# Kernel optimization log

Hardware: AMD Instinct MI355X
Metric: run time of the kernel (lower is better)

The kernel has to match this reference:

```python
import jax, jax.numpy as jnp
import numpy as np

N, C = 8, 3
HD, WD = 1024, 1280   # camera (depth) resolution
HS, WS = 800, 1280    # projector pattern resolution


def _build_calib():
    fx, fy, dx, dy = 1200.0, 1200.0, 640.0, 512.0
    ww = np.arange(WD, dtype=np.float32)[None, :].repeat(HD, 0)
    hh = np.arange(HD, dtype=np.float32)[:, None].repeat(WD, 1)
    vec = np.stack([(ww - dx) / fx, (hh - dy) / fy, np.ones_like(ww)], axis=2)  # [H,W,3]
    th = 0.15
    ext_rot = np.array([[np.cos(th), 0.0, np.sin(th)],
                        [0.0, 1.0, 0.0],
                        [-np.sin(th), 0.0, np.cos(th)]], np.float32)
    abc = np.einsum('ij,hwj->hwi', ext_rot, vec).astype(np.float32)  # [H,W,3]
    abc_mat = np.transpose(abc, (2, 0, 1))  # [3,H,W] (plb.a2t HWC->CHW)
    ext_tran = np.array([200.0, 0.0, 50.0], np.float32)
    pat_intrin = np.array([1100.0, 1100.0, 640.0, 400.0], np.float32)
    return abc_mat, ext_tran, pat_intrin


def setup_inputs() -> dict:
    key = jax.random.key(0)
    k1, k2 = jax.random.split(key)
    abc, tr, pi = _build_calib()
    depth_mat = 500.0 + 500.0 * jax.random.uniform(k1, (N, 1, HD, WD), jnp.float32)
    src_mat = jax.random.normal(k2, (N, C, HS, WS), jnp.float32)
    return {"depth_mat": depth_mat, "src_mat": src_mat,
            "abc_mat": jnp.asarray(abc), "ext_tran": jnp.asarray(tr),
            "pat_intrin": jnp.asarray(pi)}


def _grid_sample_border(src, gx, gy):
    # src: [N,C,Hs,Ws]; gx,gy: [N,H,W] normalized grid; bilinear,
    # align_corners=False, padding_mode='border' (torch semantics).
    n, c, hs, ws = src.shape
    x = ((gx + 1.0) * ws - 1.0) * 0.5
    y = ((gy + 1.0) * hs - 1.0) * 0.5
    x = jnp.clip(x, 0.0, ws - 1.0)
    y = jnp.clip(y, 0.0, hs - 1.0)
    x0 = jnp.floor(x)
    y0 = jnp.floor(y)
    wx = x - x0
    wy = y - y0
    x0i = x0.astype(jnp.int32)
    y0i = y0.astype(jnp.int32)
    x1i = jnp.minimum(x0i + 1, ws - 1)
    y1i = jnp.minimum(y0i + 1, hs - 1)
    b = jnp.arange(n)[:, None, None]

    def g(yi, xi):
        return src[b, :, yi, xi]  # [N,H,W,C]

    out = (g(y0i, x0i) * ((1.0 - wy) * (1.0 - wx))[..., None]
           + g(y0i, x1i) * ((1.0 - wy) * wx)[..., None]
           + g(y1i, x0i) * (wy * (1.0 - wx))[..., None]
           + g(y1i, x1i) * (wy * wx)[..., None])
    return jnp.transpose(out, (0, 3, 1, 2))  # [N,C,H,W]


def reference(depth_mat, src_mat, abc_mat, ext_tran, pat_intrin):
    hs, ws = src_mat.shape[-2:]
    denom = abc_mat[2] * depth_mat + ext_tran[2]          # [N,1,H,W]
    xx = (abc_mat[0] * depth_mat + ext_tran[0]) / denom
    yy = (abc_mat[1] * depth_mat + ext_tran[1]) / denom
    fu, fv, du, dv = pat_intrin
    uu = fu * xx + du
    vv = fv * yy + dv
    # NOTE: original normalizes by (size-1) even with align_corners=False;
    # replicated faithfully.
    gx = 2.0 * uu[:, 0] / (ws - 1) - 1.0                  # [N,H,W]
    gy = 2.0 * vv[:, 0] / (hs - 1) - 1.0
    return _grid_sample_border(src_mat, gx, gy)
```

## Files before the change

kernel.cpp:

```cpp
#include <hip/hip_runtime.h>

#define N_  8
#define C_  3
#define HD_ 1024
#define WD_ 1280
#define HS_ 800
#define WS_ 1280

__global__ __launch_bounds__(256) void warp_from_depth_kernel(
    const float* __restrict__ depth,
    const float* __restrict__ src,
    const float* __restrict__ abc,
    const float* __restrict__ tr,
    const float* __restrict__ pin,
    float* __restrict__ out)
{
    const int HW = HD_ * WD_;
    int idx = blockIdx.x * blockDim.x + threadIdx.x;
    if (idx >= N_ * HW) return;

    int n  = idx / HW;
    int hw = idx - n * HW;

    float d = depth[idx];
    float a = abc[hw];
    float b = abc[HW + hw];
    float c = abc[2 * HW + hw];

    float tx = tr[0], ty = tr[1], tz = tr[2];
    float fu = pin[0], fv = pin[1], du = pin[2], dv = pin[3];

    float denom = c * d + tz;
    float inv = 1.0f / denom;
    float xx = (a * d + tx) * inv;
    float yy = (b * d + ty) * inv;
    float uu = fu * xx + du;
    float vv = fv * yy + dv;

    float gx = 2.0f * uu / (float)(WS_ - 1) - 1.0f;
    float gy = 2.0f * vv / (float)(HS_ - 1) - 1.0f;
    float x = ((gx + 1.0f) * (float)WS_ - 1.0f) * 0.5f;
    float y = ((gy + 1.0f) * (float)HS_ - 1.0f) * 0.5f;

    x = fminf(fmaxf(x, 0.0f), (float)(WS_ - 1));
    y = fminf(fmaxf(y, 0.0f), (float)(HS_ - 1));

    float x0f = floorf(x);
    float y0f = floorf(y);
    float wx = x - x0f;
    float wy = y - y0f;
    int x0 = (int)x0f;
    int y0 = (int)y0f;
    int x1 = min(x0 + 1, WS_ - 1);
    int y1 = min(y0 + 1, HS_ - 1);

    float w00 = (1.0f - wy) * (1.0f - wx);
    float w01 = (1.0f - wy) * wx;
    float w10 = wy * (1.0f - wx);
    float w11 = wy * wx;

    const size_t HWs = (size_t)HS_ * WS_;
    const float* sn = src + (size_t)n * C_ * HWs;
    int o00 = y0 * WS_ + x0;
    int o01 = y0 * WS_ + x1;
    int o10 = y1 * WS_ + x0;
    int o11 = y1 * WS_ + x1;

    float* on = out + (size_t)n * C_ * HW + hw;
#pragma unroll
    for (int ch = 0; ch < C_; ++ch) {
        const float* sc = sn + (size_t)ch * HWs;
        float v = sc[o00] * w00 + sc[o01] * w01
                + sc[o10] * w10 + sc[o11] * w11;
        on[(size_t)ch * HW] = v;
    }
}

extern "C" void kernel_launch(void* const* d_in, const int* in_sizes, int n_in,
                              void* d_out, int out_size, void* d_ws, size_t ws_size,
                              hipStream_t stream) {
    const float* depth = (const float*)d_in[0];
    const float* src   = (const float*)d_in[1];
    const float* abc   = (const float*)d_in[2];
    const float* tr    = (const float*)d_in[3];
    const float* pin   = (const float*)d_in[4];
    float* out = (float*)d_out;

    const int total = N_ * HD_ * WD_;
    const int block = 256;
    const int grid = (total + block - 1) / block;
    warp_from_depth_kernel<<<grid, block, 0, stream>>>(depth, src, abc, tr, pin, out);
}
```

Before: 347.2 us.

## Pre-pack source into interleaved bf16 channels before bilinear gather

Adds a pre-pass kernel that converts the planar fp32 source image into a per-pixel interleaved bf16 layout of 8 bytes per pixel, with the three channels packed into one uint2. The main warp kernel then fetches each of the four bilinear taps with a single 8-byte load instead of twelve scattered fp32 loads across three planes. This targets gather traffic and cache-line waste in the main kernel. In exchange it adds a full read of the source and a write of the packed copy on every call, and it lowers the precision of source values to bf16, which may break tolerance. A planar fallback runs when the workspace is too small.

Measured after the change: 316.0 us. 9.0% less time.

```diff
diff --git a/kernel.cpp b/kernel.cpp
--- a/kernel.cpp
+++ b/kernel.cpp
@@ -7,9 +7,47 @@
 #define HS_ 800
 #define WS_ 1280
 
-__global__ __launch_bounds__(256) void warp_from_depth_kernel(
+__device__ __forceinline__ unsigned short f2bf(float f) {
+    unsigned int u = __float_as_uint(f);
+    unsigned int r = (u + 0x7FFFu + ((u >> 16) & 1u)) >> 16;
+    return (unsigned short)r;
+}
+__device__ __forceinline__ float bf2f(unsigned int h) {
+    return __uint_as_float(h << 16);
+}
+
+__global__ __launch_bounds__(256) void interleave_kernel(
+    const float* __restrict__ src, uint4* __restrict__ ws)
+{
+    const size_t HWs = (size_t)HS_ * WS_;
+    size_t g = (size_t)blockIdx.x * blockDim.x + threadIdx.x;
+    size_t base = g * 4;
+    if (base >= (size_t)N_ * HWs) return;
+    int n = (int)(base / HWs);
+    size_t p = base - (size_t)n * HWs;
+    const float* s = src + (size_t)n * C_ * HWs + p;
+    float4 c0 = *(const float4*)(s);
+    float4 c1 = *(const float4*)(s + HWs);
+    float4 c2 = *(const float4*)(s + 2 * HWs);
+
+    uint4 A, B;
+    A.x = (unsigned)f2bf(c0.x) | ((unsigned)f2bf(c1.x) << 16);
+    A.y = (unsigned)f2bf(c2.x);
+    A.z = (unsigned)f2bf(c0.y) | ((unsigned)f2bf(c1.y) << 16);
+    A.w = (unsigned)f2bf(c2.y);
+    B.x = (unsigned)f2bf(c0.z) | ((unsigned)f2bf(c1.z) << 16);
+    B.y = (unsigned)f2bf(c2.z);
+    B.z = (unsigned)f2bf(c0.w) | ((unsigned)f2bf(c1.w) << 16);
+    B.w = (unsigned)f2bf(c2.w);
+
+    size_t o = base / 2;
+    ws[o]     = A;
+    ws[o + 1] = B;
+}
+
+__global__ __launch_bounds__(256) void warp_main_kernel(
     const float* __restrict__ depth,
-    const float* __restrict__ src,
+    const uint2* __restrict__ wsrc,
     const float* __restrict__ abc,
     const float* __restrict__ tr,
     const float* __restrict__ pin,
@@ -60,19 +98,67 @@
     float w11 = wy * wx;
 
     const size_t HWs = (size_t)HS_ * WS_;
+    const uint2* sn = wsrc + (size_t)n * HWs;
+    uint2 t00 = sn[(size_t)y0 * WS_ + x0];
+    uint2 t01 = sn[(size_t)y0 * WS_ + x1];
+    uint2 t10 = sn[(size_t)y1 * WS_ + x0];
+    uint2 t11 = sn[(size_t)y1 * WS_ + x1];
+
+    float* on = out + (size_t)n * C_ * HW + hw;
+
+    float v0 = bf2f(t00.x & 0xFFFFu) * w00 + bf2f(t01.x & 0xFFFFu) * w01
+             + bf2f(t10.x & 0xFFFFu) * w10 + bf2f(t11.x & 0xFFFFu) * w11;
+    float v1 = bf2f(t00.x >> 16) * w00 + bf2f(t01.x >> 16) * w01
+             + bf2f(t10.x >> 16) * w10 + bf2f(t11.x >> 16) * w11;
+    float v2 = bf2f(t00.y & 0xFFFFu) * w00 + bf2f(t01.y & 0xFFFFu) * w01
+             + bf2f(t10.y & 0xFFFFu) * w10 + bf2f(t11.y & 0xFFFFu) * w11;
+
+    on[0]              = v0;
+    on[(size_t)HW]     = v1;
+    on[(size_t)2 * HW] = v2;
+}
+
+__global__ __launch_bounds__(256) void warp_planar_kernel(
+    const float* __restrict__ depth, const float* __restrict__ src,
+    const float* __restrict__ abc, const float* __restrict__ tr,
+    const float* __restrict__ pin, float* __restrict__ out)
+{
+    const int HW = HD_ * WD_;
+    int idx = blockIdx.x * blockDim.x + threadIdx.x;
+    if (idx >= N_ * HW) return;
+    int n  = idx / HW;
+    int hw = idx - n * HW;
+    float d = depth[idx];
+    float a = abc[hw];
+    float b = abc[HW + hw];
+    float c = abc[2 * HW + hw];
+    float denom = c * d + tr[2];
+    float inv = 1.0f / denom;
+    float uu = pin[0] * ((a * d + tr[0]) * inv) + pin[2];
+    float vv = pin[1] * ((b * d + tr[1]) * inv) + pin[3];
+    float gx = 2.0f * uu / (float)(WS_ - 1) - 1.0f;
+    float gy = 2.0f * vv / (float)(HS_ - 1) - 1.0f;
+    float x = ((gx + 1.0f) * (float)WS_ - 1.0f) * 0.5f;
+    float y = ((gy + 1.0f) * (float)HS_ - 1.0f) * 0.5f;
+    x = fminf(fmaxf(x, 0.0f), (float)(WS_ - 1));
+    y = fminf(fmaxf(y, 0.0f), (float)(HS_ - 1));
+    float x0f = floorf(x), y0f = floorf(y);
+    float wx = x - x0f, wy = y - y0f;
+    int x0 = (int)x0f, y0 = (int)y0f;
+    int x1 = min(x0 + 1, WS_ - 1);
+    int y1 = min(y0 + 1, HS_ - 1);
+    float w00 = (1.0f - wy) * (1.0f - wx), w01 = (1.0f - wy) * wx;
+    float w10 = wy * (1.0f - wx), w11 = wy * wx;
+    const size_t HWs = (size_t)HS_ * WS_;
     const float* sn = src + (size_t)n * C_ * HWs;
-    int o00 = y0 * WS_ + x0;
-    int o01 = y0 * WS_ + x1;
-    int o10 = y1 * WS_ + x0;
-    int o11 = y1 * WS_ + x1;
-
+    int o00 = y0 * WS_ + x0, o01 = y0 * WS_ + x1;
+    int o10 = y1 * WS_ + x0, o11 = y1 * WS_ + x1;
     float* on = out + (size_t)n * C_ * HW + hw;
 #pragma unroll
     for (int ch = 0; ch < C_; ++ch) {
         const float* sc = sn + (size_t)ch * HWs;
-        float v = sc[o00] * w00 + sc[o01] * w01
-                + sc[o10] * w10 + sc[o11] * w11;
-        on[(size_t)ch * HW] = v;
+        on[(size_t)ch * HW] = sc[o00] * w00 + sc[o01] * w01
+                            + sc[o10] * w10 + sc[o11] * w11;
     }
 }
 
@@ -86,8 +172,19 @@
     const float* pin   = (const float*)d_in[4];
     float* out = (float*)d_out;
 
+    const size_t need = (size_t)N_ * HS_ * WS_ * 8;
     const int total = N_ * HD_ * WD_;
     const int block = 256;
-    const int grid = (total + block - 1) / block;
-    warp_from_depth_kernel<<<grid, block, 0, stream>>>(depth, src, abc, tr, pin, out);
+
+    if (ws_size >= need) {
+        const size_t src_px = (size_t)N_ * HS_ * WS_;
+        const int g1 = (int)((src_px / 4 + block - 1) / block);
+        interleave_kernel<<<g1, block, 0, stream>>>(src, (uint4*)d_ws);
+        const int g2 = (total + block - 1) / block;
+        warp_main_kernel<<<g2, block, 0, stream>>>(depth, (const uint2*)d_ws,
+                                                   abc, tr, pin, out);
+    } else {
+        const int g = (total + block - 1) / block;
+        warp_planar_kernel<<<g, block, 0, stream>>>(depth, src, abc, tr, pin, out);
+    }
 }
```

## Pack source into fp16 horizontal-pair texels and gather with dot2

Applied to the files above, without the earlier changes.

Adds a pre-pass that converts the planar fp32 source into an interleaved 16-byte texel holding fp16 pairs (x, x+1) for all three channels. The main kernel then needs only two 16-byte gathers per output pixel instead of twelve scalar loads, does the blend with fdot2, and handles four pixels per thread with vector loads and nontemporal stores. This cuts scattered gather transactions, but adds a full pass over the source into workspace each call and lowers precision to fp16 for source values and weights.

Result: faster. 339.4 us (-2.2%).

```diff
diff --git a/kernel.cpp b/kernel.cpp
--- a/kernel.cpp
+++ b/kernel.cpp
@@ -7,72 +7,175 @@
 #define HS_ 800
 #define WS_ 1280
 
-__global__ __launch_bounds__(256) void warp_from_depth_kernel(
+typedef _Float16 h2_t __attribute__((ext_vector_type(2)));
+typedef float f32x4 __attribute__((ext_vector_type(4)));
+
+__device__ __forceinline__ unsigned pack_h2(float a, float b) {
+    h2_t h;
+    h.x = (_Float16)a;
+    h.y = (_Float16)b;
+    return __builtin_bit_cast(unsigned, h);
+}
+__device__ __forceinline__ h2_t as_h2(unsigned u) {
+    return __builtin_bit_cast(h2_t, u);
+}
+__device__ __forceinline__ float fdot2(h2_t a, h2_t b, float c) {
+#if __has_builtin(__builtin_amdgcn_fdot2)
+    return __builtin_amdgcn_fdot2(a, b, c, false);
+#else
+    return (float)a.x * (float)b.x + (float)a.y * (float)b.y + c;
+#endif
+}
+
+__global__ __launch_bounds__(256) void pair_pack_kernel(
+    const float* __restrict__ src, uint4* __restrict__ ws)
+{
+    const size_t HWs = (size_t)HS_ * WS_;
+    size_t g = (size_t)blockIdx.x * blockDim.x + threadIdx.x;
+    if (g >= (size_t)N_ * HWs) return;
+    int n = (int)(g / HWs);
+    size_t p = g - (size_t)n * HWs;
+    int x = (int)(p % WS_);
+    int dx = (x < WS_ - 1) ? 1 : 0;
+
+    const float* s0 = src + (size_t)n * C_ * HWs + p;
+    const float* s1 = s0 + HWs;
+    const float* s2 = s1 + HWs;
+
+    float c0a = s0[0], c0b = s0[dx];
+    float c1a = s1[0], c1b = s1[dx];
+    float c2a = s2[0], c2b = s2[dx];
+
+    uint4 e;
+    e.x = pack_h2(c0a, c0b);
+    e.y = pack_h2(c1a, c1b);
+    e.z = pack_h2(c2a, c2b);
+    e.w = 0u;
+    ws[g] = e;
+}
+
+__global__ __launch_bounds__(256) void warp_main4_kernel(
     const float* __restrict__ depth,
-    const float* __restrict__ src,
+    const uint4* __restrict__ wsrc,
     const float* __restrict__ abc,
     const float* __restrict__ tr,
     const float* __restrict__ pin,
     float* __restrict__ out)
 {
     const int HW = HD_ * WD_;
+    int t = blockIdx.x * blockDim.x + threadIdx.x;
+    int base = t * 4;
+    if (base >= N_ * HW) return;
+
+    int n  = base / HW;
+    int hw = base - n * HW;
+
+    f32x4 d4 = *(const f32x4*)(depth + base);
+    f32x4 a4 = *(const f32x4*)(abc + hw);
+    f32x4 b4 = *(const f32x4*)(abc + HW + hw);
+    f32x4 c4 = *(const f32x4*)(abc + 2 * HW + hw);
+
+    float tx = tr[0], ty = tr[1], tz = tr[2];
+    float fu = pin[0], fv = pin[1], du = pin[2], dv = pin[3];
+
+    const size_t HWs = (size_t)HS_ * WS_;
+    const uint4* sn = wsrc + (size_t)n * HWs;
+
+    f32x4 r0, r1, r2;
+
+#pragma unroll
+    for (int i = 0; i < 4; ++i) {
+        float d = d4[i];
+        float a = a4[i];
+        float b = b4[i];
+        float c = c4[i];
+
+        float denom = c * d + tz;
+        float inv = 1.0f / denom;
+        float xx = (a * d + tx) * inv;
+        float yy = (b * d + ty) * inv;
+        float uu = fu * xx + du;
+        float vv = fv * yy + dv;
+
+        float gx = 2.0f * uu / (float)(WS_ - 1) - 1.0f;
+        float gy = 2.0f * vv / (float)(HS_ - 1) - 1.0f;
+        float x = ((gx + 1.0f) * (float)WS_ - 1.0f) * 0.5f;
+        float y = ((gy + 1.0f) * (float)HS_ - 1.0f) * 0.5f;
+
+        x = fminf(fmaxf(x, 0.0f), (float)(WS_ - 1));
+        y = fminf(fmaxf(y, 0.0f), (float)(HS_ - 1));
+
+        float x0f = floorf(x);
+        float y0f = floorf(y);
+        float wx = x - x0f;
+        float wy = y - y0f;
+        int x0 = (int)x0f;
+        int y0 = (int)y0f;
+        int y1 = min(y0 + 1, HS_ - 1);
+
+        uint4 E0 = sn[(size_t)y0 * WS_ + x0];
+        uint4 E1 = sn[(size_t)y1 * WS_ + x0];
+
+        float w00 = (1.0f - wy) * (1.0f - wx);
+        float w01 = (1.0f - wy) * wx;
+        float w10 = wy * (1.0f - wx);
+        float w11 = wy * wx;
+
+        h2_t wA = { (_Float16)w00, (_Float16)w01 };
+        h2_t wB = { (_Float16)w10, (_Float16)w11 };
+
+        r0[i] = fdot2(as_h2(E0.x), wA, fdot2(as_h2(E1.x), wB, 0.0f));
+        r1[i] = fdot2(as_h2(E0.y), wA, fdot2(as_h2(E1.y), wB, 0.0f));
+        r2[i] = fdot2(as_h2(E0.z), wA, fdot2(as_h2(E1.z), wB, 0.0f));
+    }
+
+    float* on = out + (size_t)n * C_ * HW + hw;
+    __builtin_nontemporal_store(r0, (f32x4*)(on));
+    __builtin_nontemporal_store(r1, (f32x4*)(on + (size_t)HW));
+    __builtin_nontemporal_store(r2, (f32x4*)(on + (size_t)2 * HW));
+}
+
+__global__ __launch_bounds__(256) void warp_planar_kernel(
+    const float* __restrict__ depth, const float* __restrict__ src,
+    const float* __restrict__ abc, const float* __restrict__ tr,
+    const float* __restrict__ pin, float* __restrict__ out)
+{
+    const int HW = HD_ * WD_;
     int idx = blockIdx.x * blockDim.x + threadIdx.x;
     if (idx >= N_ * HW) return;
-
     int n  = idx / HW;
     int hw = idx - n * HW;
-
     float d = depth[idx];
     float a = abc[hw];
     float b = abc[HW + hw];
     float c = abc[2 * HW + hw];
-
-    float tx = tr[0], ty = tr[1], tz = tr[2];
-    float fu = pin[0], fv = pin[1], du = pin[2], dv = pin[3];
-
-    float denom = c * d + tz;
+    float denom = c * d + tr[2];
     float inv = 1.0f / denom;
-    float xx = (a * d + tx) * inv;
-    float yy = (b * d + ty) * inv;
-    float uu = fu * xx + du;
-    float vv = fv * yy + dv;
-
+    float uu = pin[0] * ((a * d + tr[0]) * inv) + pin[2];
+    float vv = pin[1] * ((b * d + tr[1]) * inv) + pin[3];
     float gx = 2.0f * uu / (float)(WS_ - 1) - 1.0f;
     float gy = 2.0f * vv / (float)(HS_ - 1) - 1.0f;
     float x = ((gx + 1.0f) * (float)WS_ - 1.0f) * 0.5f;
     float y = ((gy + 1.0f) * (float)HS_ - 1.0f) * 0.5f;
-
     x = fminf(fmaxf(x, 0.0f), (float)(WS_ - 1));
     y = fminf(fmaxf(y, 0.0f), (float)(HS_ - 1));
-
-    float x0f = floorf(x);
-    float y0f = floorf(y);
-    float wx = x - x0f;
-    float wy = y - y0f;
-    int x0 = (int)x0f;
-    int y0 = (int)y0f;
+    float x0f = floorf(x), y0f = floorf(y);
+    float wx = x - x0f, wy = y - y0f;
+    int x0 = (int)x0f, y0 = (int)y0f;
     int x1 = min(x0 + 1, WS_ - 1);
     int y1 = min(y0 + 1, HS_ - 1);
-
-    float w00 = (1.0f - wy) * (1.0f - wx);
-    float w01 = (1.0f - wy) * wx;
-    float w10 = wy * (1.0f - wx);
-    float w11 = wy * wx;
-
+    float w00 = (1.0f - wy) * (1.0f - wx), w01 = (1.0f - wy) * wx;
+    float w10 = wy * (1.0f - wx), w11 = wy * wx;
     const size_t HWs = (size_t)HS_ * WS_;
     const float* sn = src + (size_t)n * C_ * HWs;
-    int o00 = y0 * WS_ + x0;
-    int o01 = y0 * WS_ + x1;
-    int o10 = y1 * WS_ + x0;
-    int o11 = y1 * WS_ + x1;
-
+    int o00 = y0 * WS_ + x0, o01 = y0 * WS_ + x1;
+    int o10 = y1 * WS_ + x0, o11 = y1 * WS_ + x1;
     float* on = out + (size_t)n * C_ * HW + hw;
 #pragma unroll
     for (int ch = 0; ch < C_; ++ch) {
         const float* sc = sn + (size_t)ch * HWs;
-        float v = sc[o00] * w00 + sc[o01] * w01
-                + sc[o10] * w10 + sc[o11] * w11;
-        on[(size_t)ch * HW] = v;
+        on[(size_t)ch * HW] = sc[o00] * w00 + sc[o01] * w01
+                            + sc[o10] * w10 + sc[o11] * w11;
     }
 }
 
@@ -86,8 +189,19 @@
     const float* pin   = (const float*)d_in[4];
     float* out = (float*)d_out;
 
+    const size_t src_px = (size_t)N_ * HS_ * WS_;
+    const size_t need = src_px * 16;
     const int total = N_ * HD_ * WD_;
     const int block = 256;
-    const int grid = (total + block - 1) / block;
-    warp_from_depth_kernel<<<grid, block, 0, stream>>>(depth, src, abc, tr, pin, out);
-}
+
+    if (ws_size >= need) {
+        const int g1 = (int)((src_px + block - 1) / block);
+        pair_pack_kernel<<<g1, block, 0, stream>>>(src, (uint4*)d_ws);
+        const int g2 = (total / 4 + block - 1) / block;
+        warp_main4_kernel<<<g2, block, 0, stream>>>(depth, (const uint4*)d_ws,
+                                                    abc, tr, pin, out);
+    } else {
+        const int g = (total + block - 1) / block;
+        warp_planar_kernel<<<g, block, 0, stream>>>(depth, src, abc, tr, pin, out);
+    }
+}
```
